# Kernel tuning notes

Hardware: AMD Instinct MI355X
Metric: run time of the kernel (lower is better)

## Reference

```python
import jax, jax.numpy as jnp
import numpy as np

NUM_HEADS = 4
SPLIT = 2
DIM_FULL = 384  # constructor dim; scale uses dim // num_heads
SCALE = (DIM_FULL // NUM_HEADS) ** -0.5


def img2windows(img, ws, nh):
    # img: (B, D, H, W, C) -> (num_windows, nh, N, C//nh), N = prod(ws)
    B, D, H, W, C = img.shape
    d, h, w = ws
    x = img.reshape(B, D // d, d, H // h, h, W // w, w, C)
    x = x.transpose(0, 1, 3, 5, 2, 4, 6, 7).reshape(-1, d * h * w, C)
    return x.reshape(-1, d * h * w, nh, C // nh).transpose(0, 2, 1, 3)


def windows2img(xw, ws, B, D, H, W):
    # xw: (num_windows, d, h, w, C) -> (B, D, H, W, C)
    d, h, w = ws
    x = xw.reshape(B, D // d, H // h, W // w, d, h, w, -1)
    return x.transpose(0, 1, 4, 2, 5, 3, 6, 7).reshape(B, D, H, W, -1)


def setup_inputs() -> dict:
    key = jax.random.key(0)
    ks = jax.random.split(key, 5)
    B, D, H, W, C = 2, 8, 64, 64, 96
    qkv = jax.random.normal(ks[0], (3, B, D, H, W, C), jnp.float32)
    conv_w = jax.random.normal(ks[1], (C, 1, 3, 3, 3), jnp.float32) * 0.1  # depthwise Conv3d weight (O, I/groups, kD, kH, kW)
    conv_b = jax.random.normal(ks[2], (C,), jnp.float32) * 0.01
    proj_w = jax.random.normal(ks[3], (C, C), jnp.float32) * (C ** -0.5)  # torch Linear weight (out, in)
    proj_b = jax.random.normal(ks[4], (C,), jnp.float32) * 0.01
    return {"qkv": qkv, "conv_w": conv_w, "conv_b": conv_b, "proj_w": proj_w, "proj_b": proj_b}


def reference(qkv, conv_w, conv_b, proj_w, proj_b):
    q, k, v = qkv[0], qkv[1], qkv[2]
    B, D, H, W, C = q.shape
    ws = (1, H, SPLIT)  # idx == 0: (D_sp, H_sp, W_sp) = (1, H, split_size)
    qw = img2windows(q, ws, NUM_HEADS) * SCALE  # (nw, nh, N, hd)
    kw = img2windows(k, ws, NUM_HEADS)
    vw = img2windows(v, ws, NUM_HEADS)
    # LePE: depthwise 3x3x3 conv over v in NCDHW layout
    x = v.transpose(0, 4, 1, 2, 3)
    lepe = jax.lax.conv_general_dilated(
        x, conv_w, window_strides=(1, 1, 1), padding=[(1, 1)] * 3,
        dimension_numbers=("NCDHW", "OIDHW", "NCDHW"),
        feature_group_count=C) + conv_b[None, :, None, None, None]
    lepe = lepe.transpose(0, 2, 3, 4, 1)
    lepew = img2windows(lepe, ws, NUM_HEADS)
    # per-window attention
    attn = jax.nn.softmax(jnp.einsum("whnd,whmd->whnm", qw, kw), axis=-1)
    out = jnp.einsum("whnm,whmd->whnd", attn, vw) + lepew  # (nw, nh, N, hd)
    N = qw.shape[2]
    out = out.transpose(0, 2, 1, 3).reshape(-1, N, C)
    out = out @ proj_w.T + proj_b
    out = out.reshape(-1, ws[0], ws[1], ws[2], C)
    return windows2img(out, ws, B, D, H, W)
```

## Files before the change

### kernel.cpp

```cpp
#include <hip/hip_runtime.h>
#include <hip/hip_bf16.h>

constexpr int D_ = 8, H_ = 64, W_ = 64, C_ = 96;
constexpr int WC    = W_ * C_;
constexpr int HWC   = H_ * W_ * C_;
constexpr int BDHWC = 2 * D_ * HWC;
constexpr float SCALE = 0.10206207261596577f;

typedef __attribute__((ext_vector_type(4))) float f32x4;
typedef __attribute__((ext_vector_type(8))) short s16x8;

__device__ inline ushort f2bf(float x) {
  union { __hip_bfloat16 h; ushort u; } c;
  c.h = __float2bfloat16(x);
  return c.u;
}
__device__ inline float bf2f(ushort u) {
  union { float f; unsigned i; } c;
  c.i = ((unsigned)u) << 16;
  return c.f;
}
__device__ inline int xswz8(int bid, int nwg) {
  return (bid & 7) * (nwg >> 3) + (bid >> 3);
}

constexpr int QSTR = 40;
constexpr int PSTR = 136;
constexpr int OFF_Q  = 0;
constexpr int OFF_K  = 5120;
constexpr int OFF_VT = 10240;
constexpr int OFF_P  = 14592;
constexpr int LDS_HW = 32000;

__global__ void __launch_bounds__(256, 2)
attn_mfma_kernel(const float* __restrict__ qkv, float* __restrict__ out) {
  __shared__ ushort sH[LDS_HW];
  ushort* sQ  = sH + OFF_Q;
  ushort* sK  = sH + OFF_K;
  ushort* sVt = sH + OFF_VT;
  ushort* sP  = sH + OFF_P;

  const int t    = threadIdx.x;
  const int bid  = xswz8(blockIdx.x, 2048);
  const int head = bid & 3;
  const int nw   = bid >> 2;
  const int wq   = nw & 31;
  const int d    = (nw >> 5) & 7;
  const int b    = nw >> 8;
  const int hc   = head * 24;

  const float* qpl = qkv + (size_t)(b * 8 + d) * HWC;
  const float* kpl = qpl + BDHWC;
  const float* vpl = kpl + BDHWC;

  {
    const s16x8 Z = {0, 0, 0, 0, 0, 0, 0, 0};
    int row = t >> 1, col = 24 + (t & 1) * 8;
    *reinterpret_cast<s16x8*>(&sQ[row * QSTR + col]) = Z;
    *reinterpret_cast<s16x8*>(&sK[row * QSTR + col]) = Z;
    if (t < 136) *reinterpret_cast<s16x8*>(&sVt[24 * PSTR + t * 8]) = Z;
  }

  #pragma unroll
  for (int it = 0; it < 3; ++it) {
    int idx = t + it * 256;
    int tok = idx / 6, c4 = (idx - tok * 6) * 4;
    int g = (tok >> 1) * WC + (wq * 2 + (tok & 1)) * 96 + hc + c4;
    float4 qv = *reinterpret_cast<const float4*>(qpl + g);
    float4 kv = *reinterpret_cast<const float4*>(kpl + g);
    float4 vv = *reinterpret_cast<const float4*>(vpl + g);
    ushort4 qh = { f2bf(qv.x * SCALE), f2bf(qv.y * SCALE),
                   f2bf(qv.z * SCALE), f2bf(qv.w * SCALE) };
    ushort4 kh = { f2bf(kv.x), f2bf(kv.y), f2bf(kv.z), f2bf(kv.w) };
    *reinterpret_cast<ushort4*>(&sQ[tok * QSTR + c4]) = qh;
    *reinterpret_cast<ushort4*>(&sK[tok * QSTR + c4]) = kh;
    sVt[(c4 + 0) * PSTR + tok] = f2bf(vv.x);
    sVt[(c4 + 1) * PSTR + tok] = f2bf(vv.y);
    sVt[(c4 + 2) * PSTR + tok] = f2bf(vv.z);
    sVt[(c4 + 3) * PSTR + tok] = f2bf(vv.w);
  }
  __syncthreads();

  const int wv = t >> 6, lane = t & 63;
  const int lr = lane & 15;
  const int lg = lane >> 4;
  const int r0 = (2 * wv) * 16;
  const int r1 = (2 * wv + 1) * 16;

  f32x4 accS[2][8];
  #pragma unroll
  for (int i = 0; i < 2; ++i)
    #pragma unroll
    for (int j = 0; j < 8; ++j) accS[i][j] = f32x4{0.f, 0.f, 0.f, 0.f};

  {
    s16x8 a0 = *reinterpret_cast<const s16x8*>(&sQ[(r0 + lr) * QSTR + lg * 8]);
    s16x8 a1 = *reinterpret_cast<const s16x8*>(&sQ[(r1 + lr) * QSTR + lg * 8]);
    #pragma unroll
    for (int nb = 0; nb < 8; ++nb) {
      s16x8 bb = *reinterpret_cast<const s16x8*>(&sK[(nb * 16 + lr) * QSTR + lg * 8]);
      accS[0][nb] = __builtin_amdgcn_mfma_f32_16x16x32_bf16(a0, bb, accS[0][nb], 0, 0, 0);
      accS[1][nb] = __builtin_amdgcn_mfma_f32_16x16x32_bf16(a1, bb, accS[1][nb], 0, 0, 0);
    }
  }

  float rsum[2][4];
  #pragma unroll
  for (int rb = 0; rb < 2; ++rb) {
    #pragma unroll
    for (int r = 0; r < 4; ++r) {
      float s = 0.f;
      #pragma unroll
      for (int nb = 0; nb < 8; ++nb) {
        float e = __expf(accS[rb][nb][r]);
        accS[rb][nb][r] = e;
        s += e;
      }
      s += __shfl_xor(s, 1); s += __shfl_xor(s, 2);
      s += __shfl_xor(s, 4); s += __shfl_xor(s, 8);
      rsum[rb][r] = s;
    }
  }

  #pragma unroll
  for (int rb = 0; rb < 2; ++rb)
    #pragma unroll
    for (int nb = 0; nb < 8; ++nb)
      #pragma unroll
      for (int r = 0; r < 4; ++r)
        sP[((2 * wv + rb) * 16 + lg * 4 + r) * PSTR + nb * 16 + lr] =
            f2bf(accS[rb][nb][r]);
  __syncthreads();

  f32x4 accO[2][2];
  #pragma unroll
  for (int i = 0; i < 2; ++i)
    #pragma unroll
    for (int j = 0; j < 2; ++j) accO[i][j] = f32x4{0.f, 0.f, 0.f, 0.f};

  #pragma unroll
  for (int kb = 0; kb < 4; ++kb) {
    s16x8 pa0 = *reinterpret_cast<const s16x8*>(&sP[(r0 + lr) * PSTR + kb * 32 + lg * 8]);
    s16x8 pa1 = *reinterpret_cast<const s16x8*>(&sP[(r1 + lr) * PSTR + kb * 32 + lg * 8]);
    s16x8 vb0 = *reinterpret_cast<const s16x8*>(&sVt[lr * PSTR + kb * 32 + lg * 8]);
    s16x8 vb1 = *reinterpret_cast<const s16x8*>(&sVt[(16 + lr) * PSTR + kb * 32 + lg * 8]);
    accO[0][0] = __builtin_amdgcn_mfma_f32_16x16x32_bf16(pa0, vb0, accO[0][0], 0, 0, 0);
    accO[0][1] = __builtin_amdgcn_mfma_f32_16x16x32_bf16(pa0, vb1, accO[0][1], 0, 0, 0);
    accO[1][0] = __builtin_amdgcn_mfma_f32_16x16x32_bf16(pa1, vb0, accO[1][0], 0, 0, 0);
    accO[1][1] = __builtin_amdgcn_mfma_f32_16x16x32_bf16(pa1, vb1, accO[1][1], 0, 0, 0);
  }

  float* opl = out + (size_t)(b * 8 + d) * HWC;
  #pragma unroll
  for (int rb = 0; rb < 2; ++rb) {
    #pragma unroll
    for (int r = 0; r < 4; ++r) {
      int tok = (2 * wv + rb) * 16 + lg * 4 + r;
      int g = (tok >> 1) * WC + (wq * 2 + (tok & 1)) * 96 + hc;
      float inv = 1.0f / rsum[rb][r];
      opl[g + lr] = accO[rb][0][r] * inv;
      if (lr < 8) opl[g + 16 + lr] = accO[rb][1][r] * inv;
    }
  }
}

constexpr int VSTR = 104;
constexpr int WSTR = 104;

__global__ void __launch_bounds__(256, 4)
lepe_proj_fused_kernel(const float* __restrict__ qkv, const float* __restrict__ cw,
                       const float* __restrict__ cbias, const float* __restrict__ pw,
                       const float* __restrict__ pb, float* __restrict__ io) {
  __shared__ ushort sV[64 * VSTR];
  __shared__ ushort sW[96 * WSTR];
  __shared__ ushort sCW[27 * 96];
  __shared__ float  sCB[96];
  __shared__ float  sPB[96];

  const int t   = threadIdx.x;
  const int bid = xswz8(blockIdx.x, 1024);
  const int h   = bid & 63;
  const int d   = (bid >> 6) & 7;
  const int b   = bid >> 9;

  float* iop = io + (size_t)(b * 8 + d) * HWC + h * WC;
  const float* vbatch = qkv + 2 * (size_t)BDHWC + (size_t)b * 8 * HWC;

  const int tt  = t >> 2;
  const int cbk = (t & 3) * 24;

  float4 az[6];
  #pragma unroll
  for (int j = 0; j < 6; ++j)
    az[j] = *reinterpret_cast<const float4*>(iop + tt * 96 + cbk + j * 4);

  #pragma unroll
  for (int it = 0; it < 9; ++it) {
    int idx = t + it * 256;
    int co = idx / 24, c4 = (idx - co * 24) * 4;
    float4 x = *reinterpret_cast<const float4*>(pw + co * 96 + c4);
    ushort4 hx = { f2bf(x.x), f2bf(x.y), f2bf(x.z), f2bf(x.w) };
    *reinterpret_cast<ushort4*>(&sW[co * WSTR + c4]) = hx;
  }
  for (int idx = t; idx < 2592; idx += 256) {
    int c = idx / 27, tap = idx - c * 27;
    sCW[tap * 96 + c] = f2bf(cw[idx]);
  }
  if (t < 96) { sCB[t] = cbias[t]; sPB[t] = pb[t]; }

  float lep[24];
  #pragma unroll
  for (int j = 0; j < 6; ++j) {
    lep[4*j+0] = az[j].x; lep[4*j+1] = az[j].y;
    lep[4*j+2] = az[j].z; lep[4*j+3] = az[j].w;
  }

  const float fw0 = (tt > 0)  ? 1.f : 0.f;
  const float fw2 = (tt < 63) ? 1.f : 0.f;
  const int   zw0 = (tt > 0)  ? tt - 1 : 0;
  const int   zw2 = (tt < 63) ? tt + 1 : 63;

  #define TAP(zw, tap, FW)                                                   \
    {                                                                        \
      _Pragma("unroll")                                                      \
      for (int j8 = 0; j8 < 3; ++j8) {                                       \
        union { s16x8 v; ushort u[8]; } vu;                                  \
        vu.v = *reinterpret_cast<const s16x8*>(&sV[(zw) * VSTR + cbk + j8 * 8]); \
        union { s16x8 v; ushort u[8]; } wu;                                  \
        wu.v = *reinterpret_cast<const s16x8*>(&sCW[(tap) * 96 + cbk + j8 * 8]); \
        _Pragma("unroll")                                                    \
        for (int e = 0; e < 8; ++e)                                          \
          lep[8*j8+e] = fmaf(bf2f(vu.u[e]) * (FW), bf2f(wu.u[e]), lep[8*j8+e]); \
      }                                                                      \
    }

  #pragma unroll
  for (int dd = 0; dd < 3; ++dd) {
    int zd = d + dd - 1;
    if (zd < 0 || zd >= D_) continue;
    #pragma unroll
    for (int dh = 0; dh < 3; ++dh) {
      int zh = h + dh - 1;
      if (zh < 0 || zh >= H_) continue;
      __syncthreads();
      {
        const float4* src = reinterpret_cast<const float4*>(
            vbatch + (size_t)zd * HWC + zh * WC);
        #pragma unroll
        for (int it = 0; it < 6; ++it) {
          int idx = t + it * 256;
          int tok = idx / 24, c4 = idx - tok * 24;
          float4 x = src[idx];
          ushort4 hx = { f2bf(x.x), f2bf(x.y), f2bf(x.z), f2bf(x.w) };
          *reinterpret_cast<ushort4*>(&sV[tok * VSTR + c4 * 4]) = hx;
        }
      }
      __syncthreads();
      const int tap0 = dd * 9 + dh * 3;
      TAP(zw0, tap0 + 0, fw0);
      TAP(tt,  tap0 + 1, 1.f);
      TAP(zw2, tap0 + 2, fw2);
    }
  }
  #undef TAP

  __syncthreads();
  #pragma unroll
  for (int j = 0; j < 6; ++j) {
    float4 bz = *reinterpret_cast<const float4*>(sCB + cbk + j * 4);
    ushort4 hx = { f2bf(lep[4*j+0] + bz.x), f2bf(lep[4*j+1] + bz.y),
                   f2bf(lep[4*j+2] + bz.z), f2bf(lep[4*j+3] + bz.w) };
    *reinterpret_cast<ushort4*>(&sV[tt * VSTR + cbk + j * 4]) = hx;
  }
  __syncthreads();

  const int wv = t >> 6, lane = t & 63;
  const int lr = lane & 15, lg = lane >> 4;

  f32x4 acc[6];
  #pragma unroll
  for (int cb = 0; cb < 6; ++cb) {
    float bv = sPB[cb * 16 + lr];
    acc[cb] = f32x4{bv, bv, bv, bv};
  }
  s16x8 afr[3];
  #pragma unroll
  for (int kb = 0; kb < 3; ++kb)
    afr[kb] = *reinterpret_cast<const s16x8*>(&sV[(wv * 16 + lr) * VSTR + kb * 32 + lg * 8]);
  #pragma unroll
  for (int kb = 0; kb < 3; ++kb) {
    #pragma unroll
    for (int cb = 0; cb < 6; ++cb) {
      s16x8 bfr = *reinterpret_cast<const s16x8*>(&sW[(cb * 16 + lr) * WSTR + kb * 32 + lg * 8]);
      acc[cb] = __builtin_amdgcn_mfma_f32_16x16x32_bf16(afr[kb], bfr, acc[cb], 0, 0, 0);
    }
  }

  #pragma unroll
  for (int cb = 0; cb < 6; ++cb) {
    #pragma unroll
    for (int r = 0; r < 4; ++r) {
      int tok = wv * 16 + lg * 4 + r;
      iop[tok * 96 + cb * 16 + lr] = acc[cb][r];
    }
  }
}

extern "C" void kernel_launch(void* const* d_in, const int* in_sizes, int n_in,
                              void* d_out, int out_size, void* d_ws, size_t ws_size,
                              hipStream_t stream) {
  const float* qkv = (const float*)d_in[0];
  const float* cw  = (const float*)d_in[1];
  const float* cb  = (const float*)d_in[2];
  const float* pw  = (const float*)d_in[3];
  const float* pb  = (const float*)d_in[4];
  float* out = (float*)d_out;

  hipLaunchKernelGGL(attn_mfma_kernel, dim3(2048), dim3(256), 0, stream, qkv, out);
  hipLaunchKernelGGL(lepe_proj_fused_kernel, dim3(1024), dim3(256), 0, stream,
                     qkv, cw, cb, pw, pb, out);
}
```

Measured before the change: 63.47 us.

## Load Q directly to registers and split attention into two key halves

Q is now loaded from global memory straight into MFMA A-operand registers, with zero padding for the unused K lanes, instead of being staged through shared memory. The score/softmax/PV computation is split into two 64-key halves, which halves the accumulator registers and the P buffer in LDS. The launch bound rises from 2 to 4 blocks per SM to raise occupancy. In exchange there is an extra barrier per half, and the Q global loads are now 8-float strided per lane.

```diff
diff --git a/kernel.cpp b/kernel.cpp
--- a/kernel.cpp
+++ b/kernel.cpp
@@ -24,21 +24,15 @@
   return (bid & 7) * (nwg >> 3) + (bid >> 3);
 }
 
-constexpr int QSTR = 40;
-constexpr int PSTR = 136;
-constexpr int OFF_Q  = 0;
-constexpr int OFF_K  = 5120;
-constexpr int OFF_VT = 10240;
-constexpr int OFF_P  = 14592;
-constexpr int LDS_HW = 32000;
-
-__global__ void __launch_bounds__(256, 2)
+constexpr int QSTR  = 40;
+constexpr int PSTR  = 136;
+constexpr int PSTR2 = 72;
+
+__global__ void __launch_bounds__(256, 4)
 attn_mfma_kernel(const float* __restrict__ qkv, float* __restrict__ out) {
-  __shared__ ushort sH[LDS_HW];
-  ushort* sQ  = sH + OFF_Q;
-  ushort* sK  = sH + OFF_K;
-  ushort* sVt = sH + OFF_VT;
-  ushort* sP  = sH + OFF_P;
+  __shared__ ushort sK[128 * QSTR];
+  __shared__ ushort sVt[32 * PSTR];
+  __shared__ ushort sP[128 * PSTR2];
 
   const int t    = threadIdx.x;
   const int bid  = xswz8(blockIdx.x, 2048);
@@ -56,7 +50,6 @@
   {
     const s16x8 Z = {0, 0, 0, 0, 0, 0, 0, 0};
     int row = t >> 1, col = 24 + (t & 1) * 8;
-    *reinterpret_cast<s16x8*>(&sQ[row * QSTR + col]) = Z;
     *reinterpret_cast<s16x8*>(&sK[row * QSTR + col]) = Z;
     if (t < 136) *reinterpret_cast<s16x8*>(&sVt[24 * PSTR + t * 8]) = Z;
   }
@@ -66,20 +59,15 @@
     int idx = t + it * 256;
     int tok = idx / 6, c4 = (idx - tok * 6) * 4;
     int g = (tok >> 1) * WC + (wq * 2 + (tok & 1)) * 96 + hc + c4;
-    float4 qv = *reinterpret_cast<const float4*>(qpl + g);
     float4 kv = *reinterpret_cast<const float4*>(kpl + g);
     float4 vv = *reinterpret_cast<const float4*>(vpl + g);
-    ushort4 qh = { f2bf(qv.x * SCALE), f2bf(qv.y * SCALE),
-                   f2bf(qv.z * SCALE), f2bf(qv.w * SCALE) };
     ushort4 kh = { f2bf(kv.x), f2bf(kv.y), f2bf(kv.z), f2bf(kv.w) };
-    *reinterpret_cast<ushort4*>(&sQ[tok * QSTR + c4]) = qh;
     *reinterpret_cast<ushort4*>(&sK[tok * QSTR + c4]) = kh;
     sVt[(c4 + 0) * PSTR + tok] = f2bf(vv.x);
     sVt[(c4 + 1) * PSTR + tok] = f2bf(vv.y);
     sVt[(c4 + 2) * PSTR + tok] = f2bf(vv.z);
     sVt[(c4 + 3) * PSTR + tok] = f2bf(vv.w);
   }
-  __syncthreads();
 
   const int wv = t >> 6, lane = t & 63;
   const int lr = lane & 15;
@@ -87,77 +75,107 @@
   const int r0 = (2 * wv) * 16;
   const int r1 = (2 * wv + 1) * 16;
 
-  f32x4 accS[2][8];
+  s16x8 a0 = {0,0,0,0,0,0,0,0}, a1 = {0,0,0,0,0,0,0,0};
+  if (lg < 3) {
+    union { s16x8 v; ushort u[8]; } qa;
+    int tok = r0 + lr;
+    const float* qp = qpl + (tok >> 1) * WC + (wq * 2 + (tok & 1)) * 96 + hc + lg * 8;
+    float4 x0 = *reinterpret_cast<const float4*>(qp);
+    float4 x1 = *reinterpret_cast<const float4*>(qp + 4);
+    qa.u[0] = f2bf(x0.x * SCALE); qa.u[1] = f2bf(x0.y * SCALE);
+    qa.u[2] = f2bf(x0.z * SCALE); qa.u[3] = f2bf(x0.w * SCALE);
+    qa.u[4] = f2bf(x1.x * SCALE); qa.u[5] = f2bf(x1.y * SCALE);
+    qa.u[6] = f2bf(x1.z * SCALE); qa.u[7] = f2bf(x1.w * SCALE);
+    a0 = qa.v;
+    tok = r1 + lr;
+    qp = qpl + (tok >> 1) * WC + (wq * 2 + (tok & 1)) * 96 + hc + lg * 8;
+    x0 = *reinterpret_cast<const float4*>(qp);
+    x1 = *reinterpret_cast<const float4*>(qp + 4);
+    qa.u[0] = f2bf(x0.x * SCALE); qa.u[1] = f2bf(x0.y * SCALE);
+    qa.u[2] = f2bf(x0.z * SCALE); qa.u[3] = f2bf(x0.w * SCALE);
+    qa.u[4] = f2bf(x1.x * SCALE); qa.u[5] = f2bf(x1.y * SCALE);
+    qa.u[6] = f2bf(x1.z * SCALE); qa.u[7] = f2bf(x1.w * SCALE);
+    a1 = qa.v;
+  }
+
+  __syncthreads();
+
+  float rsum[2][4];
+  #pragma unroll
+  for (int rb = 0; rb < 2; ++rb)
+    #pragma unroll
+    for (int r = 0; r < 4; ++r) rsum[rb][r] = 0.f;
+
+  f32x4 accO[2][2];
   #pragma unroll
   for (int i = 0; i < 2; ++i)
     #pragma unroll
-    for (int j = 0; j < 8; ++j) accS[i][j] = f32x4{0.f, 0.f, 0.f, 0.f};
-
-  {
-    s16x8 a0 = *reinterpret_cast<const s16x8*>(&sQ[(r0 + lr) * QSTR + lg * 8]);
-    s16x8 a1 = *reinterpret_cast<const s16x8*>(&sQ[(r1 + lr) * QSTR + lg * 8]);
-    #pragma unroll
-    for (int nb = 0; nb < 8; ++nb) {
-      s16x8 bb = *reinterpret_cast<const s16x8*>(&sK[(nb * 16 + lr) * QSTR + lg * 8]);
+    for (int j = 0; j < 2; ++j) accO[i][j] = f32x4{0.f, 0.f, 0.f, 0.f};
+
+  #pragma unroll
+  for (int half = 0; half < 2; ++half) {
+    f32x4 accS[2][4];
+    #pragma unroll
+    for (int i = 0; i < 2; ++i)
+      #pragma unroll
+      for (int j = 0; j < 4; ++j) accS[i][j] = f32x4{0.f, 0.f, 0.f, 0.f};
+
+    #pragma unroll
+    for (int nb = 0; nb < 4; ++nb) {
+      s16x8 bb = *reinterpret_cast<const s16x8*>(
+          &sK[(half * 64 + nb * 16 + lr) * QSTR + lg * 8]);
       accS[0][nb] = __builtin_amdgcn_mfma_f32_16x16x32_bf16(a0, bb, accS[0][nb], 0, 0, 0);
       accS[1][nb] = __builtin_amdgcn_mfma_f32_16x16x32_bf16(a1, bb, accS[1][nb], 0, 0, 0);
     }
-  }
-
-  float rsum[2][4];
+
+    #pragma unroll
+    for (int rb = 0; rb < 2; ++rb)
+      #pragma unroll
+      for (int nb = 0; nb < 4; ++nb)
+        #pragma unroll
+        for (int r = 0; r < 4; ++r) {
+          float e = __expf(accS[rb][nb][r]);
+          accS[rb][nb][r] = e;
+          rsum[rb][r] += e;
+        }
+
+    if (half) __syncthreads();
+
+    #pragma unroll
+    for (int rb = 0; rb < 2; ++rb)
+      #pragma unroll
+      for (int nb = 0; nb < 4; ++nb)
+        #pragma unroll
+        for (int r = 0; r < 4; ++r)
+          sP[((2 * wv + rb) * 16 + lg * 4 + r) * PSTR2 + nb * 16 + lr] =
+              f2bf(accS[rb][nb][r]);
+    __syncthreads();
+
+    #pragma unroll
+    for (int kb = 0; kb < 2; ++kb) {
+      int kc = half * 64 + kb * 32 + lg * 8;
+      s16x8 pa0 = *reinterpret_cast<const s16x8*>(&sP[(r0 + lr) * PSTR2 + kb * 32 + lg * 8]);
+      s16x8 pa1 = *reinterpret_cast<const s16x8*>(&sP[(r1 + lr) * PSTR2 + kb * 32 + lg * 8]);
+      s16x8 vb0 = *reinterpret_cast<const s16x8*>(&sVt[lr * PSTR + kc]);
+      s16x8 vb1 = *reinterpret_cast<const s16x8*>(&sVt[(16 + lr) * PSTR + kc]);
+      accO[0][0] = __builtin_amdgcn_mfma_f32_16x16x32_bf16(pa0, vb0, accO[0][0], 0, 0, 0);
+      accO[0][1] = __builtin_amdgcn_mfma_f32_16x16x32_bf16(pa0, vb1, accO[0][1], 0, 0, 0);
+      accO[1][0] = __builtin_amdgcn_mfma_f32_16x16x32_bf16(pa1, vb0, accO[1][0], 0, 0, 0);
+      accO[1][1] = __builtin_amdgcn_mfma_f32_16x16x32_bf16(pa1, vb1, accO[1][1], 0, 0, 0);
+    }
+  }
+
+  float* opl = out + (size_t)(b * 8 + d) * HWC;
   #pragma unroll
   for (int rb = 0; rb < 2; ++rb) {
     #pragma unroll
     for (int r = 0; r < 4; ++r) {
-      float s = 0.f;
-      #pragma unroll
-      for (int nb = 0; nb < 8; ++nb) {
-        float e = __expf(accS[rb][nb][r]);
-        accS[rb][nb][r] = e;
-        s += e;
-      }
+      float s = rsum[rb][r];
       s += __shfl_xor(s, 1); s += __shfl_xor(s, 2);
       s += __shfl_xor(s, 4); s += __shfl_xor(s, 8);
-      rsum[rb][r] = s;
-    }
-  }
-
-  #pragma unroll
-  for (int rb = 0; rb < 2; ++rb)
-    #pragma unroll
-    for (int nb = 0; nb < 8; ++nb)
-      #pragma unroll
-      for (int r = 0; r < 4; ++r)
-        sP[((2 * wv + rb) * 16 + lg * 4 + r) * PSTR + nb * 16 + lr] =
-            f2bf(accS[rb][nb][r]);
-  __syncthreads();
-
-  f32x4 accO[2][2];
-  #pragma unroll
-  for (int i = 0; i < 2; ++i)
-    #pragma unroll
-    for (int j = 0; j < 2; ++j) accO[i][j] = f32x4{0.f, 0.f, 0.f, 0.f};
-
-  #pragma unroll
-  for (int kb = 0; kb < 4; ++kb) {
-    s16x8 pa0 = *reinterpret_cast<const s16x8*>(&sP[(r0 + lr) * PSTR + kb * 32 + lg * 8]);
-    s16x8 pa1 = *reinterpret_cast<const s16x8*>(&sP[(r1 + lr) * PSTR + kb * 32 + lg * 8]);
-    s16x8 vb0 = *reinterpret_cast<const s16x8*>(&sVt[lr * PSTR + kb * 32 + lg * 8]);
-    s16x8 vb1 = *reinterpret_cast<const s16x8*>(&sVt[(16 + lr) * PSTR + kb * 32 + lg * 8]);
-    accO[0][0] = __builtin_amdgcn_mfma_f32_16x16x32_bf16(pa0, vb0, accO[0][0], 0, 0, 0);
-    accO[0][1] = __builtin_amdgcn_mfma_f32_16x16x32_bf16(pa0, vb1, accO[0][1], 0, 0, 0);
-    accO[1][0] = __builtin_amdgcn_mfma_f32_16x16x32_bf16(pa1, vb0, accO[1][0], 0, 0, 0);
-    accO[1][1] = __builtin_amdgcn_mfma_f32_16x16x32_bf16(pa1, vb1, accO[1][1], 0, 0, 0);
-  }
-
-  float* opl = out + (size_t)(b * 8 + d) * HWC;
-  #pragma unroll
-  for (int rb = 0; rb < 2; ++rb) {
-    #pragma unroll
-    for (int r = 0; r < 4; ++r) {
       int tok = (2 * wv + rb) * 16 + lg * 4 + r;
       int g = (tok >> 1) * WC + (wq * 2 + (tok & 1)) * 96 + hc;
-      float inv = 1.0f / rsum[rb][r];
+      float inv = 1.0f / s;
       opl[g + lr] = accO[rb][0][r] * inv;
       if (lr < 8) opl[g + 16 + lr] = accO[rb][1][r] * inv;
     }
```

New measurement: 62.03 us. 2.3% less time.
